# Performance work log

Hardware: AMD Instinct MI355X
Metric: run time of the kernel (lower is better)

Reference implementation:

```python
import jax, jax.numpy as jnp
import numpy as np

B, N, C, D = 2, 6, 64, 40
FH, FW = 12, 33
IMG_H, IMG_W = 384, 1056
NX, NY, NZ = 100, 100, 4
LOWER = np.array([-50.0, -50.0, -10.0], np.float32)   # xbound[0], ybound[0], zbound[0]
DXV = np.array([1.0, 1.0, 5.0], np.float32)           # voxel sizes


def _conv(x, w, pad):
    return jax.lax.conv_general_dilated(x, w, (1, 1), [(pad, pad), (pad, pad)],
                                        dimension_numbers=('NCHW', 'OIHW', 'NCHW'))


def _bn(x, s, b):
    return x * s[None, :, None, None] + b[None, :, None, None]


def _se(x, w1, b1, w2, b2):
    m = x.mean((2, 3))                                   # global avg pool -> (B, C)
    g = jax.nn.sigmoid(jax.nn.silu(m @ w1.T + b1) @ w2.T + b2)
    return x * g[:, :, None, None]


def _frustum():
    ds = jnp.arange(4.0, 44.0, 1.0)                      # (D,) depth bins
    xs = jnp.linspace(0.0, IMG_W - 1.0, FW)
    ys = jnp.linspace(0.0, IMG_H - 1.0, FH)
    f = jnp.stack(jnp.broadcast_arrays(xs[None, None, :], ys[None, :, None], ds[:, None, None]), -1)
    return f.reshape(-1, 3)                              # (D*FH*FW, 3) in (x_px, y_px, depth)


def reference(feats, rots, trans, intrinsics, nw1, bn1s, bn1b, se1w1, se1b1, se1w2, se1b2,
              nw2, bn2s, bn2b, dhw, dhb, chw, chb, bcw1, bcs1, bcb1, bcsw1, bcsb1, bcsw2,
              bcsb2, bcw2, bcs2, bcb2, dw1, ds1, db1, dw2, db2):
    BN = B * N
    # ---- CamEncoderV2 neck + heads (backbone 1280ch@1/32 features given directly) ----
    x = jax.nn.silu(_bn(_conv(feats, nw1, 0), bn1s, bn1b))
    x = _se(x, se1w1, se1b1, se1w2, se1b2)
    x = jax.nn.silu(_bn(_conv(x, nw2, 1), bn2s, bn2b))
    depth = jax.nn.softmax(_conv(x, dhw, 0) + dhb[None, :, None, None], axis=1)  # (BN, D, FH, FW)
    ctx = _conv(x, chw, 0) + chb[None, :, None, None]                            # (BN, C, FH, FW)
    # ---- geometry: pixel frustum -> ego-frame points ----
    rots_f = rots.reshape(BN, 3, 3)
    trans_f = trans.reshape(BN, 3)
    K = intrinsics.reshape(BN, 3, 3)
    pts = _frustum()                                     # (P0, 3), P0 = D*FH*FW
    d = pts[:, 2]
    fx, fy = K[:, 0, 0][:, None], K[:, 1, 1][:, None]
    cx, cy = K[:, 0, 2][:, None], K[:, 1, 2][:, None]
    cam = jnp.stack([(pts[None, :, 0] - cx) * d[None, :] / fx,
                     (pts[None, :, 1] - cy) * d[None, :] / fy,
                     jnp.broadcast_to(d[None, :], (BN, d.shape[0]))], -1)        # (BN, P0, 3)
    geom = jnp.einsum('bij,bpj->bpi', rots_f, cam) + trans_f[:, None, :]
    geom = geom.reshape(B, -1, 3)                        # (B, N*P0, 3)
    # ---- lift: outer product context x depth ----
    ff = (ctx[:, None, :, :, :] * depth[:, :, None, :, :])                       # (BN, D, C, FH, FW)
    ff = ff.transpose(0, 1, 3, 4, 2).reshape(B, -1, C)                           # (B, N*P0, C)
    # ---- splat: voxel pooling (scatter-add into BEV grid) ----
    idx = jnp.floor((geom - jnp.asarray(LOWER)) / jnp.asarray(DXV)).astype(jnp.int32)
    valid = jnp.all((idx >= 0) & (idx < jnp.array([NX, NY, NZ])), axis=-1)
    sid = idx[..., 2] * (NX * NY) + idx[..., 0] * NY + idx[..., 1]
    sid = jnp.where(valid, sid, 0)
    ffm = ff * valid[..., None]
    pooled = jax.vmap(lambda f, i: jax.ops.segment_sum(f, i, num_segments=NZ * NX * NY))(ffm, sid)
    bev = pooled.reshape(B, NZ, NX, NY, C).transpose(0, 1, 4, 2, 3).reshape(B, NZ * C, NX, NY)
    # ---- BEVCompressorV2 (residual conv-SE-conv) ----
    h = jax.nn.relu(_bn(_conv(bev, bcw1, 1), bcs1, bcb1))
    h = _se(h, bcsw1, bcsb1, bcsw2, bcsb2)
    h = jax.nn.relu(_bn(_conv(h, bcw2, 1), bcs2, bcb2))
    bev = bev + h
    # ---- decoder ----
    h = jax.nn.relu(_bn(_conv(bev, dw1, 1), ds1, db1))
    out = _conv(h, dw2, 0) + db2[None, :, None, None]    # (B, nz*num_classes, NX, NY)
    return out.reshape(B, 4, NZ, NX, NY)


def setup_inputs():
    f32 = jnp.float32
    ks = jax.random.split(jax.random.key(0), 16)
    feats = jax.random.normal(ks[0], (B * N, 1280, FH, FW), f32) * 0.5
    # cam->ego: z_cam -> x_ego, -x_cam -> y_ego, -y_cam -> z_ego, plus per-camera yaw
    Rbase = np.array([[0., 0., 1.], [-1., 0., 0.], [0., -1., 0.]], np.float32)
    yaw = np.deg2rad(np.arange(N) * 60.0).astype(np.float32)
    c, s = np.cos(yaw), np.sin(yaw)
    Rz = np.zeros((N, 3, 3), np.float32)
    Rz[:, 0, 0] = c; Rz[:, 0, 1] = -s; Rz[:, 1, 0] = s; Rz[:, 1, 1] = c; Rz[:, 2, 2] = 1.0
    rots = jnp.asarray(np.broadcast_to(np.einsum('nij,jk->nik', Rz, Rbase), (B, N, 3, 3)).copy())
    trans = jax.random.normal(ks[1], (B, N, 3), f32) * 1.0
    K = np.array([[800., 0., 528.], [0., 800., 192.], [0., 0., 1.]], np.float32)
    intrinsics = jnp.asarray(np.broadcast_to(K, (B, N, 3, 3)).copy())

    def w(k, shape, fan_in):
        return jax.random.normal(k, shape, f32) * np.float32(np.sqrt(2.0 / fan_in))

    kk = jax.random.split(ks[2], 16)
    return dict(
        feats=feats, rots=rots, trans=trans, intrinsics=intrinsics,
        nw1=w(kk[0], (256, 1280, 1, 1), 1280), bn1s=jnp.ones(256, f32), bn1b=jnp.zeros(256, f32),
        se1w1=w(kk[1], (32, 256), 256), se1b1=jnp.zeros(32, f32),
        se1w2=w(kk[2], (256, 32), 32), se1b2=jnp.zeros(256, f32),
        nw2=w(kk[3], (256, 256, 3, 3), 2304), bn2s=jnp.ones(256, f32), bn2b=jnp.zeros(256, f32),
        dhw=w(kk[4], (40, 256, 1, 1), 256), dhb=jnp.zeros(40, f32),
        chw=w(kk[5], (64, 256, 1, 1), 256), chb=jnp.zeros(64, f32),
        bcw1=w(kk[6], (256, 256, 3, 3), 2304), bcs1=jnp.ones(256, f32), bcb1=jnp.zeros(256, f32),
        bcsw1=w(kk[7], (16, 256), 256), bcsb1=jnp.zeros(16, f32),
        bcsw2=w(kk[8], (256, 16), 16), bcsb2=jnp.zeros(256, f32),
        bcw2=w(kk[9], (256, 256, 3, 3), 2304), bcs2=jnp.ones(256, f32), bcb2=jnp.zeros(256, f32),
        dw1=w(kk[10], (128, 256, 3, 3), 2304), ds1=jnp.ones(128, f32), db1=jnp.zeros(128, f32),
        dw2=w(kk[11], (16, 128, 1, 1), 128), db2=jnp.zeros(16, f32),
    )
```

## Files before the change

### kernel.cpp

```cpp
#include <hip/hip_runtime.h>
#include <hip/hip_bf16.h>
#include <cmath>


typedef __attribute__((ext_vector_type(8))) short short8;
typedef __attribute__((ext_vector_type(4))) float floatx4;
typedef __hip_bfloat16 hb;

__device__ __forceinline__ float sigf(float x){ return 1.0f/(1.0f+expf(-x)); }
__device__ __forceinline__ float siluf(float x){ return x*sigf(x); }
__device__ __forceinline__ void split2(float v, hb* h, hb* l){
  hb hv = __float2bfloat16(v);
  *h = hv; *l = __float2bfloat16(v - __bfloat162float(hv));
}

__global__ __launch_bounds__(256) void k_trans_featsP(
    const float* __restrict__ feats, hb* __restrict__ Fph, hb* __restrict__ Fpl)
{
  __shared__ float tile[64][65];
  int n = blockIdx.z;
  int p0 = blockIdx.x*64;
  int c0 = blockIdx.y*64;
  int tid = threadIdx.x;
  int tr = tid >> 6;
  int tc = tid & 63;
  #pragma unroll
  for (int it=0; it<16; ++it){
    int ci = c0 + it*4 + tr;
    int p = p0 + tc;
    float v = 0.f;
    if (p < 396) v = feats[((size_t)n*1280 + ci)*396 + p];
    tile[it*4+tr][tc] = v;
  }
  __syncthreads();
  #pragma unroll
  for (int iter=0; iter<2; ++iter){
    int idx = iter*256 + tid;
    int oc = idx >> 6;
    int pl = idx & 63;
    int p = p0 + pl;
    if (p < 396){
      int P = n*396 + p;
      int T = P >> 4, mm = P & 15;
      int kb = (c0 >> 5) + (oc >> 2);
      int q = oc & 3;
      int lane = q*16 + mm;
      size_t o = (((size_t)T*40 + kb)*64 + lane)*8;
      #pragma unroll
      for (int j=0; j<8; ++j){
        hb hv, lv; split2(tile[oc*8+j][pl], &hv, &lv);
        Fph[o+j] = hv; Fpl[o+j] = lv;
      }
    }
  }
}

__global__ __launch_bounds__(256) void k_wpackE(
    const float* __restrict__ nw1, const float* __restrict__ nw2,
    hb* __restrict__ Wc1h, hb* __restrict__ Wc1l,
    hb* __restrict__ Wc2h, hb* __restrict__ Wc2l)
{
  int i = blockIdx.x*256 + threadIdx.x;
  if (i < 327680){
    int j = i & 7;
    int lane = (i>>3) & 63;
    int t2 = i >> 9;
    int nb = t2 & 15;
    int kb = t2 >> 4;
    int ci = kb*32 + (lane>>4)*8 + j;
    int co = nb*16 + (lane&15);
    hb hv, lv; split2(nw1[(size_t)co*1280 + ci], &hv, &lv);
    Wc1h[i] = hv; Wc1l[i] = lv;
  } else {
    int i2 = i - 327680;
    if (i2 >= 589824) return;
    int j = i2 & 7;
    int t1 = i2 >> 3;
    int lane = t1 & 63;
    int t2 = t1 >> 6;
    int nb = t2 % 16;
    int t3 = t2 / 16;
    int tap = t3 % 9;
    int kb = t3 / 9;
    int ci = kb*32 + (lane>>4)*8 + j;
    int co = nb*16 + (lane&15);
    hb hv, lv; split2(nw2[(size_t)co*2304 + ci*9 + tap], &hv, &lv);
    Wc2h[i2] = hv; Wc2l[i2] = lv;
  }
}

__global__ __launch_bounds__(256) void k_wpackT3(
    const float* __restrict__ bcw1, const float* __restrict__ bcw2,
    const float* __restrict__ dw1,
    hb* __restrict__ W1h, hb* __restrict__ W1l,
    hb* __restrict__ W2h, hb* __restrict__ W2l,
    hb* __restrict__ W3h, hb* __restrict__ W3l)
{
  int gi = blockIdx.x*256 + threadIdx.x;
  const float* W; hb* Wh; hb* Wl; int NB; int i;
  if (gi < 589824){ W = bcw1; Wh = W1h; Wl = W1l; NB = 16; i = gi; }
  else if (gi < 1179648){ W = bcw2; Wh = W2h; Wl = W2l; NB = 16; i = gi - 589824; }
  else if (gi < 1474560){ W = dw1; Wh = W3h; Wl = W3l; NB = 8; i = gi - 1179648; }
  else return;
  int j = i & 7;
  int t1 = i >> 3;
  int lane = t1 & 63;
  int t2 = t1 >> 6;
  int nb = t2 % NB;
  int t3 = t2 / NB;
  int tap = t3 % 9;
  int kb = t3 / 9;
  int ci = kb*32 + (lane>>4)*8 + j;
  int co = nb*16 + (lane&15);
  hb hv, lv; split2(W[(size_t)co*2304 + ci*9 + tap], &hv, &lv);
  Wh[i] = hv; Wl[i] = lv;
}

__global__ __launch_bounds__(256) void k_wpackH(
    const float* __restrict__ dhw, const float* __restrict__ chw,
    hb* __restrict__ Wph, hb* __restrict__ Wpl)
{
  int i = blockIdx.x*256 + threadIdx.x;
  if (i >= 8*7*512) return;
  int j = i & 7;
  int t1 = i >> 3;
  int lane = t1 & 63;
  int t2 = t1 >> 6;
  int nb = t2 % 7;
  int kb = t2 / 7;
  int ci = kb*32 + (lane>>4)*8 + j;
  int co = nb*16 + (lane&15);
  float w = 0.f;
  if (co < 40) w = dhw[(size_t)co*256 + ci];
  else if (co < 104) w = chw[(size_t)(co-40)*256 + ci];
  hb hv, lv; split2(w, &hv, &lv);
  Wph[i] = hv; Wpl[i] = lv;
}

__global__ __launch_bounds__(256) void k_mfma_gemm1(
    const hb* __restrict__ Fph, const hb* __restrict__ Fpl,
    const hb* __restrict__ Wph, const hb* __restrict__ Wpl,
    const float* __restrict__ bns, const float* __restrict__ bnb,
    float* __restrict__ out)
{
  __shared__ short8 lbh[256], lbl[256];
  int tid = threadIdx.x;
  int wv = tid >> 6, lane = tid & 63;
  int cog = blockIdx.y;
  int Pbase = blockIdx.x*128 + wv*32;
  int q = lane >> 4;
  int T0 = blockIdx.x*8 + wv*2; if (T0 > 296) T0 = 296;
  int T1 = T0 + 1;              if (T1 > 296) T1 = 296;
  size_t a0 = (size_t)T0*2560 + lane;
  size_t a1 = (size_t)T1*2560 + lane;
  const short8* gAh = (const short8*)(const void*)Fph;
  const short8* gAl = (const short8*)(const void*)Fpl;
  const short8* gWh = (const short8*)(const void*)Wph;
  const short8* gWl = (const short8*)(const void*)Wpl;
  size_t sb = (size_t)(cog*4 + wv)*64 + lane;
  floatx4 acc[2][4];
  #pragma unroll
  for (int i=0;i<2;++i)
    #pragma unroll
    for (int j=0;j<4;++j) acc[i][j] = (floatx4)(0.f);
  short8 ph = gWh[sb], pw = gWl[sb];
  short8 cah0 = gAh[a0], cal0 = gAl[a0], cah1 = gAh[a1], cal1 = gAl[a1];
  for (int kb=0; kb<40; ++kb){
    __syncthreads();
    lbh[tid] = ph; lbl[tid] = pw;
    int nx = (kb+1 < 40) ? kb+1 : 39;
    ph = gWh[(size_t)nx*1024 + sb]; pw = gWl[(size_t)nx*1024 + sb];
    __syncthreads();
    short8 nah0 = gAh[a0 + (size_t)nx*64];
    short8 nal0 = gAl[a0 + (size_t)nx*64];
    short8 nah1 = gAh[a1 + (size_t)nx*64];
    short8 nal1 = gAl[a1 + (size_t)nx*64];
    #pragma unroll
    for (int nb=0; nb<4; ++nb){
      short8 bh = lbh[nb*64 + lane];
      short8 bl = lbl[nb*64 + lane];
      acc[0][nb] = __builtin_amdgcn_mfma_f32_16x16x32_bf16(cah0, bh, acc[0][nb], 0,0,0);
      acc[0][nb] = __builtin_amdgcn_mfma_f32_16x16x32_bf16(cah0, bl, acc[0][nb], 0,0,0);
      acc[0][nb] = __builtin_amdgcn_mfma_f32_16x16x32_bf16(cal0, bh, acc[0][nb], 0,0,0);
      acc[1][nb] = __builtin_amdgcn_mfma_f32_16x16x32_bf16(cah1, bh, acc[1][nb], 0,0,0);
      acc[1][nb] = __builtin_amdgcn_mfma_f32_16x16x32_bf16(cah1, bl, acc[1][nb], 0,0,0);
      acc[1][nb] = __builtin_amdgcn_mfma_f32_16x16x32_bf16(cal1, bh, acc[1][nb], 0,0,0);
    }
    cah0 = nah0; cal0 = nal0; cah1 = nah1; cal1 = nal1;
  }
  int n16 = lane & 15;
  #pragma unroll
  for (int mg=0; mg<2; ++mg){
    #pragma unroll
    for (int nb=0; nb<4; ++nb){
      int co = cog*64 + nb*16 + n16;
      float s = bns[co], bv = bnb[co];
      #pragma unroll
      for (int r=0; r<4; ++r){
        int P = Pbase + mg*16 + q*4 + r;
        if (P < 4752) out[(size_t)P*256 + co] = siluf(acc[mg][nb][r]*s + bv);
      }
    }
  }
}

__global__ __launch_bounds__(256) void k_meanse(
    const float* __restrict__ x1, const float* __restrict__ w1, const float* __restrict__ b1,
    const float* __restrict__ w2, const float* __restrict__ b2, float* __restrict__ g)
{
  __shared__ float m[256];
  __shared__ float h[32];
  int n = blockIdx.x; int t = threadIdx.x;
  float s = 0.f;
  for (int p=0; p<396; ++p) s += x1[((size_t)n*396+p)*256 + t];
  m[t] = s*(1.f/396.f);
  __syncthreads();
  if (t < 32){
    float s2 = b1[t];
    for (int c=0; c<256; ++c) s2 += m[c]*w1[t*256+c];
    h[t] = siluf(s2);
  }
  __syncthreads();
  float s3 = b2[t];
  for (int j=0; j<32; ++j) s3 += h[j]*w2[t*32+j];
  g[n*256+t] = sigf(s3);
}

__global__ __launch_bounds__(256) void k_se_fc(
    const float* __restrict__ mean, const float* __restrict__ w1, const float* __restrict__ b1,
    const float* __restrict__ w2, const float* __restrict__ b2, float* __restrict__ g, int H)
{
  __shared__ float m[256];
  __shared__ float h[32];
  int n = blockIdx.x; int t = threadIdx.x;
  m[t] = mean[n*256 + t];
  __syncthreads();
  if (t < H){
    float s = b1[t];
    for (int c=0; c<256; ++c) s += m[c]*w1[t*256+c];
    h[t] = siluf(s);
  }
  __syncthreads();
  float s = b2[t];
  for (int j=0; j<H; ++j) s += h[j]*w2[t*H+j];
  g[n*256+t] = sigf(s);
}

__global__ __launch_bounds__(256) void k_topad(
    const float* __restrict__ x1, const float* __restrict__ g,
    hb* __restrict__ Xh, hb* __restrict__ Xl)
{
  int y = blockIdx.x;
  int n = blockIdx.y;
  int c = threadIdx.x;
  float gc = g[n*256+c];
  for (int xx=0; xx<35; ++xx){
    float v = 0.f;
    if (y>=1 && y<=12 && xx>=1 && xx<=33)
      v = x1[((size_t)n*396 + (y-1)*33 + (xx-1))*256 + c]*gc;
    hb hv, lv; split2(v, &hv, &lv);
    size_t o = (((size_t)n*14+y)*35+xx)*256 + c;
    Xh[o] = hv; Xl[o] = lv;
  }
}

__global__ __launch_bounds__(256) void k_conv3_img(
    const hb* __restrict__ Xh, const hb* __restrict__ Xl,
    const hb* __restrict__ Wph, const hb* __restrict__ Wpl,
    const float* __restrict__ bns, const float* __restrict__ bnb,
    hb* __restrict__ outh, hb* __restrict__ outl)
{
  __shared__ __align__(16) short sAh[10*18*44];
  __shared__ __align__(16) short sAl[10*18*44];
  __shared__ short8 lbh[2][256], lbl[2][256];
  int tid = threadIdx.x;
  int wv = tid >> 6, lane = tid & 63;
  int xg = blockIdx.x;
  int n = blockIdx.y >> 1, yg = blockIdx.y & 1;
  int cog = blockIdx.z;
  int x0 = xg*16;
  int y0 = yg*8 + wv;
  int m = lane & 15, q = lane >> 4;
  floatx4 acc[2][4];
  #pragma unroll
  for (int i=0;i<2;++i)
    #pragma unroll
    for (int j=0;j<4;++j) acc[i][j] = (floatx4)(0.f);

  const short8* gAh = (const short8*)(const void*)Xh;
  const short8* gAl = (const short8*)(const void*)Xl;
  const short8* gWh = (const short8*)(const void*)Wph;
  const short8* gWl = (const short8*)(const void*)Wpl;
  const size_t sb = (size_t)(cog*4 + wv)*64 + lane;
  const size_t nbase = (size_t)n*14*35*32;

  short8 ph = gWh[sb], pl = gWl[sb];
  int cur = 0;

  for (int kb=0; kb<8; ++kb){
    #pragma unroll 3
    for (int tap=0; tap<9; ++tap){
      int idx2 = kb*9 + tap;
      if (tap == 0){
        __syncthreads();
        for (int i = tid; i < 720; i += 256){
          int rc = i >> 2, part = i & 3;
          int r = rc / 18, c2 = rc % 18;
          int yr = yg*8 + r; if (yr > 13) yr = 13;
          int xc = x0 + c2;  if (xc > 34) xc = 34;
          size_t so = nbase + (size_t)(yr*35 + xc)*32 + kb*4 + part;
          short8 vh = gAh[so], vl = gAl[so];
          int dst = (r*18 + c2)*44 + part*8;
          *(short8*)(sAh + dst) = vh;
          *(short8*)(sAl + dst) = vl;
        }
      }
      lbh[cur][tid] = ph; lbl[cur][tid] = pl;
      int nx = (idx2+1 < 72) ? idx2+1 : 71;
      ph = gWh[(size_t)nx*1024 + sb];
      pl = gWl[(size_t)nx*1024 + sb];
      __syncthreads();
      int dy = (tap*11) >> 5;
      int dx = tap - dy*3;
      int cc = dx + m;
      int a0 = ((wv + dy)*18 + cc)*44 + q*8;
      int a1 = ((wv + 4 + dy)*18 + cc)*44 + q*8;
      short8 cah0 = *(const short8*)(sAh + a0);
      short8 cal0 = *(const short8*)(sAl + a0);
      short8 cah1 = *(const short8*)(sAh + a1);
      short8 cal1 = *(const short8*)(sAl + a1);
      #pragma unroll
      for (int nb=0; nb<4; ++nb){
        short8 bh = lbh[cur][nb*64 + lane];
        short8 bl = lbl[cur][nb*64 + lane];
        acc[0][nb] = __builtin_amdgcn_mfma_f32_16x16x32_bf16(cah0, bh, acc[0][nb], 0,0,0);
        acc[0][nb] = __builtin_amdgcn_mfma_f32_16x16x32_bf16(cah0, bl, acc[0][nb], 0,0,0);
        acc[0][nb] = __builtin_amdgcn_mfma_f32_16x16x32_bf16(cal0, bh, acc[0][nb], 0,0,0);
        acc[1][nb] = __builtin_amdgcn_mfma_f32_16x16x32_bf16(cah1, bh, acc[1][nb], 0,0,0);
        acc[1][nb] = __builtin_amdgcn_mfma_f32_16x16x32_bf16(cah1, bl, acc[1][nb], 0,0,0);
        acc[1][nb] = __builtin_amdgcn_mfma_f32_16x16x32_bf16(cal1, bh, acc[1][nb], 0,0,0);
      }
      cur ^= 1;
    }
  }

  int n16 = lane & 15;
  #pragma unroll
  for (int mg=0; mg<2; ++mg){
    int oy = y0 + mg*4;
    if (oy < 12){
      #pragma unroll
      for (int r=0; r<4; ++r){
        int ox = x0 + q*4 + r;
        if (ox < 33){
          int P = n*396 + oy*33 + ox;
          #pragma unroll
          for (int nb=0; nb<4; ++nb){
            int co = cog*64 + nb*16 + n16;
            float v = siluf(acc[mg][nb][r]*bns[co] + bnb[co]);
            hb hv, lv; split2(v, &hv, &lv);
            outh[(size_t)P*256 + co] = hv;
            outl[(size_t)P*256 + co] = lv;
          }
        }
      }
    }
  }
}

__global__ __launch_bounds__(256) void k_headsM(
    const hb* __restrict__ x2h, const hb* __restrict__ x2l,
    const hb* __restrict__ Whh, const hb* __restrict__ Whl,
    const float* __restrict__ dhb, const float* __restrict__ chb,
    float* __restrict__ dep, float* __restrict__ ctx2)
{
  __shared__ short8 lbh[256], lbl[256];
  int tid = threadIdx.x;
  int wv = tid >> 6, lane = tid & 63;
  int cog = blockIdx.y;
  int nb0 = cog*4;
  int nbN = cog ? 3 : 4;
  int Pbase = blockIdx.x*128 + wv*32;
  int m = lane & 15, q = lane >> 4;
  int P0 = Pbase + m;      if (P0 > 4751) P0 = 4751;
  int P1 = Pbase + 16 + m; if (P1 > 4751) P1 = 4751;
  size_t rA0 = (size_t)P0*32 + q;
  size_t rA1 = (size_t)P1*32 + q;
  const short8* gAh = (const short8*)(const void*)x2h;
  const short8* gAl = (const short8*)(const void*)x2l;
  const short8* gWh = (const short8*)(const void*)Whh;
  const short8* gWl = (const short8*)(const void*)Whl;
  floatx4 acc[2][4];
  #pragma unroll
  for (int i=0;i<2;++i)
    #pragma unroll
    for (int j=0;j<4;++j) acc[i][j] = (floatx4)(0.f);
  for (int kb=0; kb<8; ++kb){
    __syncthreads();
    for (int i=tid; i<nbN*64; i+=256){
      lbh[i] = gWh[(size_t)(kb*7 + nb0)*64 + i];
      lbl[i] = gWl[(size_t)(kb*7 + nb0)*64 + i];
    }
    __syncthreads();
    short8 ah0 = gAh[rA0 + kb*4], al0 = gAl[rA0 + kb*4];
    short8 ah1 = gAh[rA1 + kb*4], al1 = gAl[rA1 + kb*4];
    for (int nb=0; nb<nbN; ++nb){
      short8 bh = lbh[nb*64 + lane];
      short8 bl = lbl[nb*64 + lane];
      acc[0][nb] = __builtin_amdgcn_mfma_f32_16x16x32_bf16(ah0, bh, acc[0][nb], 0,0,0);
      acc[0][nb] = __builtin_amdgcn_mfma_f32_16x16x32_bf16(ah0, bl, acc[0][nb], 0,0,0);
      acc[0][nb] = __builtin_amdgcn_mfma_f32_16x16x32_bf16(al0, bh, acc[0][nb], 0,0,0);
      acc[1][nb] = __builtin_amdgcn_mfma_f32_16x16x32_bf16(ah1, bh, acc[1][nb], 0,0,0);
      acc[1][nb] = __builtin_amdgcn_mfma_f32_16x16x32_bf16(ah1, bl, acc[1][nb], 0,0,0);
      acc[1][nb] = __builtin_amdgcn_mfma_f32_16x16x32_bf16(al1, bh, acc[1][nb], 0,0,0);
    }
  }
  int n16 = lane & 15;
  #pragma unroll
  for (int mg=0; mg<2; ++mg){
    #pragma unroll
    for (int r=0; r<4; ++r){
      int P = Pbase + mg*16 + q*4 + r;
      if (P < 4752){
        int nn = P/396, pim = P%396;
        for (int nb=0; nb<nbN; ++nb){
          int co = cog*64 + nb*16 + n16;
          float v = acc[mg][nb][r];
          if (co < 40)
            dep[((size_t)nn*40 + co)*396 + pim] = v + dhb[co];
          else if (co < 104)
            ctx2[((size_t)nn*396 + pim)*64 + (co-40)] = v + chb[co-40];
        }
      }
    }
  }
}

__global__ __launch_bounds__(256) void k_softmax40(float* __restrict__ dep)
{
  int i = blockIdx.x*256 + threadIdx.x;
  if (i >= 12*396) return;
  int n = i/396, p = i%396;
  float* base = dep + (size_t)n*40*396 + p;
  float mx = -1e30f;
  for (int d=0; d<40; ++d) mx = fmaxf(mx, base[(size_t)d*396]);
  float s = 0.f;
  for (int d=0; d<40; ++d){ float e = expf(base[(size_t)d*396]-mx); base[(size_t)d*396]=e; s+=e; }
  float inv = 1.f/s;
  for (int d=0; d<40; ++d) base[(size_t)d*396] *= inv;
}

__global__ __launch_bounds__(256) void k_geom(
    const float* __restrict__ rots, const float* __restrict__ trans,
    const float* __restrict__ intr, int* __restrict__ vox, int* __restrict__ cnt)
{
  int pt = blockIdx.x*256 + threadIdx.x;
  if (pt >= 190080) return;
  int b = pt/95040; int r = pt%95040;
  int n = r/15840;  int r2 = r%15840;
  int d = r2/396;   int pim = r2%396;
  int y = pim/33, x = pim%33;
  int bn = b*6+n;
  const float* R = rots + (size_t)bn*9;
  const float* T = trans + (size_t)bn*3;
  const float* K = intr + (size_t)bn*9;
  float fx=K[0], cx=K[2], fy=K[4], cy=K[5];
  float xs = (float)x * 32.96875f;
  float ys = (float)((double)y * (383.0/11.0));
  float dv = 4.0f + (float)d;
  float camx = (xs-cx)*dv/fx;
  float camy = (ys-cy)*dv/fy;
  float gx = R[0]*camx + R[1]*camy + R[2]*dv + T[0];
  float gy = R[3]*camx + R[4]*camy + R[5]*dv + T[1];
  float gz = R[6]*camx + R[7]*camy + R[8]*dv + T[2];
  int ix = (int)floorf(gx + 50.f);
  int iy = (int)floorf(gy + 50.f);
  int iz = (int)floorf((gz + 10.f)/5.f);
  bool valid = (ix>=0 && ix<100 && iy>=0 && iy<100 && iz>=0 && iz<4);
  int sid = iz*10000 + ix*100 + iy;
  vox[pt] = valid ? sid : -1;
  if (valid) atomicAdd(&cnt[b*40000 + sid], 1);
}

__global__ __launch_bounds__(256) void k_scan1(
    const int* __restrict__ cnt, int* __restrict__ off, int* __restrict__ bsum)
{
  __shared__ int s[256];
  int t = threadIdx.x;
  int i = blockIdx.x*256 + t;
  int v = (i < 80000) ? cnt[i] : 0;
  s[t] = v; __syncthreads();
  for (int o=1;o<256;o<<=1){
    int x = (t>=o) ? s[t-o] : 0;
    __syncthreads();
    s[t] += x;
    __syncthreads();
  }
  if (i < 80000) off[i] = s[t] - v;
  if (t == 255) bsum[blockIdx.x] = s[255];
}

__global__ void k_scan2(int* __restrict__ bsum, int nblk)
{
  if (threadIdx.x==0 && blockIdx.x==0){
    int run = 0;
    for (int j=0;j<nblk;++j){ int t = bsum[j]; bsum[j] = run; run += t; }
  }
}

__global__ __launch_bounds__(256) void k_scan3(
    int* __restrict__ off, const int* __restrict__ bsum, int* __restrict__ cur)
{
  int i = blockIdx.x*256 + threadIdx.x;
  if (i >= 80000) return;
  int o = off[i] + bsum[i>>8];
  off[i] = o;
  cur[i] = o;
}

__global__ __launch_bounds__(256) void k_fill(
    const int* __restrict__ vox, int* __restrict__ cur, int* __restrict__ list)
{
  int pt = blockIdx.x*256 + threadIdx.x;
  if (pt >= 190080) return;
  int s = vox[pt];
  if (s < 0) return;
  int b = pt/95040;
  int slot = atomicAdd(&cur[b*40000 + s], 1);
  list[slot] = pt;
}

__global__ __launch_bounds__(256) void k_zero_ring(hb* __restrict__ Ah, hb* __restrict__ Al)
{
  int i = blockIdx.x*256 + threadIdx.x;
  if (i >= 2*404*256) return;
  int c = i & 255;
  int t = i >> 8;
  int b = t / 404;
  int ridx = t % 404;
  int py, px;
  if (ridx < 102){ py = 0; px = ridx; }
  else if (ridx < 204){ py = 101; px = ridx-102; }
  else if (ridx < 304){ py = ridx-204+1; px = 0; }
  else { py = ridx-304+1; px = 101; }
  size_t o = (((size_t)b*102 + py)*102 + px)*256 + c;
  hb z = __float2bfloat16(0.f);
  Ah[o] = z; Al[o] = z;
}

__global__ __launch_bounds__(256) void k_gather(
    const int* __restrict__ off, const int* __restrict__ cnt, const int* __restrict__ list,
    const float* __restrict__ ctx2, const float* __restrict__ dep, float* __restrict__ bev,
    hb* __restrict__ Ah, hb* __restrict__ Al)
{
  int tid = threadIdx.x;
  int bv = blockIdx.x*4 + (tid>>6);
  int c = tid & 63;
  int b = bv/40000, sid = bv%40000;
  int st = off[bv], nn = cnt[bv];
  float s = 0.f;
  for (int k=0;k<nn;++k){
    int pt = list[st+k];
    int r = pt%95040;
    int bn = b*6 + r/15840;
    int r2 = r%15840;
    int dd = r2/396, pim = r2%396;
    s += ctx2[((size_t)bn*396+pim)*64 + c] * dep[((size_t)bn*40+dd)*396 + pim];
  }
  int iz = sid/10000, rem = sid%10000;
  bev[(size_t)b*2560000 + (size_t)iz*640000 + (size_t)c*10000 + rem] = s;
  int ix = rem/100, iy = rem%100;
  size_t oh = (((size_t)b*102 + (ix+1))*102 + (iy+1))*256 + iz*64 + c;
  hb hv, lv; split2(s, &hv, &lv);
  Ah[oh] = hv; Al[oh] = lv;
}

__global__ __launch_bounds__(256) void k_tohwc2(
    const float* __restrict__ in, hb* __restrict__ Ah, hb* __restrict__ Al,
    const float* __restrict__ g)
{
  __shared__ float tile[32*105];
  int py = blockIdx.x;
  int b  = blockIdx.y;
  int cg = blockIdx.z;
  int tid = threadIdx.x;
  bool inner = (py >= 1 && py <= 100);
  if (inner){
    if (tid < 64){ int cil = tid & 31; int col = (tid>>5) ? 101 : 0; tile[cil*105 + col] = 0.f; }
    for (int i = tid; i < 3200; i += 256){
      int cil = i / 100, x = i % 100;
      int ci = cg*32 + cil;
      tile[cil*105 + (x+1)] = in[(((size_t)b*256 + ci)*100 + (py-1))*100 + x];
    }
  }
  __syncthreads();
  for (int i = tid; i < 32*102; i += 256){
    int px = i >> 5, cil = i & 31;
    int ci = cg*32 + cil;
    float v = 0.f;
    if (inner){
      v = tile[cil*105 + px];
      if (g) v *= g[b*256 + ci];
    }
    hb hv, lv; split2(v, &hv, &lv);
    size_t o = (((size_t)b*102 + py)*102 + px)*256 + ci;
    Ah[o] = hv; Al[o] = lv;
  }
}

__global__ __launch_bounds__(256) void k_rowmean(
    const float* __restrict__ in, float* __restrict__ out, int rowlen, float inv)
{
  __shared__ float ws[4];
  int row = blockIdx.x; int t = threadIdx.x;
  const float* p = in + (size_t)row*rowlen;
  float s = 0.f;
  for (int i=t; i<rowlen; i+=256) s += p[i];
  #pragma unroll
  for (int off=32; off; off>>=1) s += __shfl_down(s, off);
  if ((t&63)==0) ws[t>>6] = s;
  __syncthreads();
  if (t==0) out[row] = (ws[0]+ws[1]+ws[2]+ws[3]) * inv;
}

__global__ __launch_bounds__(256) void k_conv3_bevm(
    const hb* __restrict__ Ah, const hb* __restrict__ Al,
    const hb* __restrict__ Wph, const hb* __restrict__ Wpl,
    const float* __restrict__ bns, const float* __restrict__ bnb,
    const float* __restrict__ res, float* __restrict__ out, int Cout, int NBG)
{
  __shared__ __align__(16) short sAh[10*18*44];
  __shared__ __align__(16) short sAl[10*18*44];
  __shared__ short8 lbh[2][256], lbl[2][256];
  const int NB = Cout >> 4;
  int tid = threadIdx.x;
  int wv = tid >> 6, lane = tid & 63;
  int L = blockIdx.x;
  int spatial = L / (NBG*2);
  int rem = L % (NBG*2);
  int cog = rem % NBG;
  int bb  = rem / NBG;
  int xg = spatial % 7, yg = spatial / 7;
  int x0 = xg*16;
  int y0 = yg*8 + wv;
  int m = lane & 15, q = lane >> 4;
  int nb0 = cog*4;
  floatx4 acc[2][4];
  #pragma unroll
  for (int i=0;i<2;++i)
    #pragma unroll
    for (int j=0;j<4;++j) acc[i][j] = (floatx4)(0.f);

  const short8* gAh = (const short8*)(const void*)Ah;
  const short8* gAl = (const short8*)(const void*)Al;
  const short8* gWh = (const short8*)(const void*)Wph;
  const short8* gWl = (const short8*)(const void*)Wpl;
  const size_t nbstride = (size_t)NB*64;
  const size_t sb = (size_t)(nb0 + wv)*64 + lane;

  short8 ph = gWh[sb], pl = gWl[sb];
  int cur = 0;

  for (int kb=0; kb<8; ++kb){
    #pragma unroll 3
    for (int tap=0; tap<9; ++tap){
      int idx2 = kb*9 + tap;
      if (tap == 0){
        __syncthreads();
        for (int i = tid; i < 720; i += 256){
          int rc = i >> 2, part = i & 3;
          int r = rc / 18, c = rc % 18;
          int yr = yg*8 + r; if (yr > 101) yr = 101;
          int xc = x0 + c;   if (xc > 101) xc = 101;
          size_t so = ((size_t)((bb*102 + yr)*102 + xc))*32 + kb*4 + part;
          short8 vh = gAh[so], vl = gAl[so];
          int dst = (r*18 + c)*44 + part*8;
          *(short8*)(sAh + dst) = vh;
          *(short8*)(sAl + dst) = vl;
        }
      }
      lbh[cur][tid] = ph; lbl[cur][tid] = pl;
      int nx = (idx2+1 < 72) ? idx2+1 : 71;
      ph = gWh[(size_t)nx*nbstride + sb];
      pl = gWl[(size_t)nx*nbstride + sb];
      __syncthreads();
      int dy = (tap*11) >> 5;
      int dx = tap - dy*3;
      int cc = dx + m;
      int a0 = ((wv + dy)*18 + cc)*44 + q*8;
      int a1 = ((wv + 4 + dy)*18 + cc)*44 + q*8;
      short8 cah0 = *(const short8*)(sAh + a0);
      short8 cal0 = *(const short8*)(sAl + a0);
      short8 cah1 = *(const short8*)(sAh + a1);
      short8 cal1 = *(const short8*)(sAl + a1);
      #pragma unroll
      for (int nb=0; nb<4; ++nb){
        short8 bh = lbh[cur][nb*64 + lane];
        short8 bl = lbl[cur][nb*64 + lane];
        acc[0][nb] = __builtin_amdgcn_mfma_f32_16x16x32_bf16(cah0, bh, acc[0][nb], 0,0,0);
        acc[0][nb] = __builtin_amdgcn_mfma_f32_16x16x32_bf16(cah0, bl, acc[0][nb], 0,0,0);
        acc[0][nb] = __builtin_amdgcn_mfma_f32_16x16x32_bf16(cal0, bh, acc[0][nb], 0,0,0);
        acc[1][nb] = __builtin_amdgcn_mfma_f32_16x16x32_bf16(cah1, bh, acc[1][nb], 0,0,0);
        acc[1][nb] = __builtin_amdgcn_mfma_f32_16x16x32_bf16(cah1, bl, acc[1][nb], 0,0,0);
        acc[1][nb] = __builtin_amdgcn_mfma_f32_16x16x32_bf16(cal1, bh, acc[1][nb], 0,0,0);
      }
      cur ^= 1;
    }
  }

  int n = lane & 15;
  int xq = x0 + q*4;
  #pragma unroll
  for (int mg=0; mg<2; ++mg){
    int yo = y0 + mg*4;
    if (yo < 100 && xq < 100){
      #pragma unroll
      for (int nb=0; nb<4; ++nb){
        int co = cog*64 + nb*16 + n;
        float s = bns[co], bv = bnb[co];
        floatx4 a = acc[mg][nb];
        float4 v;
        v.x = fmaxf(a[0]*s+bv, 0.f);
        v.y = fmaxf(a[1]*s+bv, 0.f);
        v.z = fmaxf(a[2]*s+bv, 0.f);
        v.w = fmaxf(a[3]*s+bv, 0.f);
        size_t o = ((size_t)(bb*Cout+co)*100 + yo)*100 + xq;
        if (res){
          float4 rv = *(const float4*)(res + o);
          v.x += rv.x; v.y += rv.y; v.z += rv.z; v.w += rv.w;
        }
        *(float4*)(out + o) = v;
      }
    }
  }
}

__global__ __launch_bounds__(256) void k_final2(
    const float* __restrict__ h, const float* __restrict__ W, const float* __restrict__ bias,
    float* __restrict__ out)
{
  __shared__ float wsl[2048];
  __shared__ float bs[16];
  int tid = threadIdx.x;
  int b = blockIdx.y;
  for (int i=tid; i<2048; i+=256) wsl[i] = W[i];
  if (tid < 16) bs[tid] = bias[tid];
  __syncthreads();
  int pix = blockIdx.x*256 + tid;
  if (pix >= 10000) return;
  float acc[16];
  #pragma unroll
  for (int oc=0; oc<16; ++oc) acc[oc] = bs[oc];
  const float* hb_ = h + (size_t)b*128*10000 + pix;
  for (int ci=0; ci<128; ++ci){
    float hv = hb_[(size_t)ci*10000];
    #pragma unroll
    for (int oc=0; oc<16; ++oc) acc[oc] += hv * wsl[oc*128 + ci];
  }
  #pragma unroll
  for (int oc=0; oc<16; ++oc)
    out[((size_t)(b*16+oc))*10000 + pix] = acc[oc];
}

extern "C" void kernel_launch(void* const* d_in, const int* in_sizes, int n_in,
                              void* d_out, int out_size, void* d_ws, size_t ws_size,
                              hipStream_t stream)
{
  (void)in_sizes; (void)n_in; (void)out_size; (void)ws_size;
  const float* feats = (const float*)d_in[0];
  const float* rots  = (const float*)d_in[1];
  const float* trans = (const float*)d_in[2];
  const float* intr  = (const float*)d_in[3];
  const float* nw1   = (const float*)d_in[4];
  const float* bn1s  = (const float*)d_in[5];
  const float* bn1b  = (const float*)d_in[6];
  const float* se1w1 = (const float*)d_in[7];
  const float* se1b1 = (const float*)d_in[8];
  const float* se1w2 = (const float*)d_in[9];
  const float* se1b2 = (const float*)d_in[10];
  const float* nw2   = (const float*)d_in[11];
  const float* bn2s  = (const float*)d_in[12];
  const float* bn2b  = (const float*)d_in[13];
  const float* dhw   = (const float*)d_in[14];
  const float* dhb   = (const float*)d_in[15];
  const float* chw   = (const float*)d_in[16];
  const float* chb   = (const float*)d_in[17];
  const float* bcw1  = (const float*)d_in[18];
  const float* bcs1  = (const float*)d_in[19];
  const float* bcb1  = (const float*)d_in[20];
  const float* bcsw1 = (const float*)d_in[21];
  const float* bcsb1 = (const float*)d_in[22];
  const float* bcsw2 = (const float*)d_in[23];
  const float* bcsb2 = (const float*)d_in[24];
  const float* bcw2  = (const float*)d_in[25];
  const float* bcs2  = (const float*)d_in[26];
  const float* bcb2  = (const float*)d_in[27];
  const float* dw1   = (const float*)d_in[28];
  const float* ds1   = (const float*)d_in[29];
  const float* db1   = (const float*)d_in[30];
  const float* dw2   = (const float*)d_in[31];
  const float* db2   = (const float*)d_in[32];
  float* out = (float*)d_out;

  float* ws = (float*)d_ws;
  float* bev   = ws;
  float* h1    = ws + 5120000;
  hb*    Ah    = (hb*)(ws + 10240000);
  hb*    Al    = (hb*)(ws + 12903424);
  float* x2    = ws + 15566848;
  float* S5    = ws + 16783360;
  float* dep   = ws + 17373184;
  float* ctx2  = ws + 17563264;
  float* mean1 = ws + 17867392;
  float* g1    = mean1 + 3072;
  float* mean2 = g1 + 3072;
  float* g2    = mean2 + 512;
  int*   vox   = (int*)(ws + 17875584);
  hb* Fph  = (hb*)bev;
  hb* Wc1h = (hb*)(bev + 3041280);
  hb* Wc1l = (hb*)(bev + 3205120);
  float* x1 = h1;
  hb* Fpl  = (hb*)(h1 + 1216512);
  hb* Xh   = (hb*)Ah;
  hb* Xl   = (hb*)Al;
  hb* Wc2h = (hb*)S5;
  hb* Wc2l = (hb*)(S5 + 294912);
  hb* x2h  = (hb*)x2;
  hb* x2l  = (hb*)(x2 + 608256);
  hb* Whh  = (hb*)S5;
  hb* Whl  = (hb*)(S5 + 14336);
  int* cnt  = (int*)h1;
  int* off  = cnt + 80000;
  int* cur  = off + 80000;
  int* bsum = cur + 80000;
  int* list = bsum + 1024;
  float* h3 = h1;
  hb* Wp1h = (hb*)x2;
  hb* Wp1l = (hb*)(x2 + 294912);
  hb* Wp3h = (hb*)(x2 + 589824);
  hb* Wp3l = (hb*)(x2 + 589824 + 147456);
  hb* Wp2h = (hb*)S5;
  hb* Wp2l = (hb*)(S5 + 294912);

  k_trans_featsP<<<dim3(7,20,12),256,0,stream>>>(feats,Fph,Fpl);
  k_wpackE<<<3584,256,0,stream>>>(nw1,nw2,Wc1h,Wc1l,Wc2h,Wc2l);
  k_mfma_gemm1<<<dim3(38,4),256,0,stream>>>(Fph,Fpl,Wc1h,Wc1l,bn1s,bn1b,x1);
  k_meanse<<<12,256,0,stream>>>(x1,se1w1,se1b1,se1w2,se1b2,g1);
  k_topad<<<dim3(14,12),256,0,stream>>>(x1,g1,Xh,Xl);
  k_conv3_img<<<dim3(3,24,4),256,0,stream>>>(Xh,Xl,Wc2h,Wc2l,bn2s,bn2b,x2h,x2l);
  k_wpackH<<<112,256,0,stream>>>(dhw,chw,Whh,Whl);
  k_headsM<<<dim3(38,2),256,0,stream>>>(x2h,x2l,Whh,Whl,dhb,chb,dep,ctx2);
  k_softmax40<<<19,256,0,stream>>>(dep);

  k_wpackT3<<<5760,256,0,stream>>>(bcw1,bcw2,dw1,Wp1h,Wp1l,Wp2h,Wp2l,Wp3h,Wp3l);

  hipMemsetAsync(cnt, 0, 80000*sizeof(int), stream);
  k_geom<<<(190080+255)/256,256,0,stream>>>(rots,trans,intr,vox,cnt);
  k_scan1<<<313,256,0,stream>>>(cnt,off,bsum);
  k_scan2<<<1,64,0,stream>>>(bsum,313);
  k_scan3<<<(80000+255)/256,256,0,stream>>>(off,bsum,cur);
  k_fill<<<(190080+255)/256,256,0,stream>>>(vox,cur,list);
  k_zero_ring<<<808,256,0,stream>>>(Ah,Al);
  k_gather<<<20000,256,0,stream>>>(off,cnt,list,ctx2,dep,bev,Ah,Al);

  k_conv3_bevm<<<728,256,0,stream>>>(Ah,Al,Wp1h,Wp1l,bcs1,bcb1,nullptr,h1,256,4);
  k_rowmean<<<512,256,0,stream>>>(h1,mean2,10000,1e-4f);
  k_se_fc<<<2,256,0,stream>>>(mean2,bcsw1,bcsb1,bcsw2,bcsb2,g2,16);
  k_tohwc2<<<dim3(102,2,8),256,0,stream>>>(h1,Ah,Al,g2);
  k_conv3_bevm<<<728,256,0,stream>>>(Ah,Al,Wp2h,Wp2l,bcs2,bcb2,bev,bev,256,4);
  k_tohwc2<<<dim3(102,2,8),256,0,stream>>>(bev,Ah,Al,nullptr);
  k_conv3_bevm<<<364,256,0,stream>>>(Ah,Al,Wp3h,Wp3l,ds1,db1,nullptr,h3,128,2);
  k_final2<<<dim3(40,2),256,0,stream>>>(h3,dw2,db2,out);
}
```

Measured before the change: 671.5 us.

## Split conv3 BEV waves by channel pairs, drop LDS weight staging; warp-parallel block scan

The 3x3 BEV conv kernel now gives each wave 4 output rows by 2 channel blocks, so each wave loads its own weight fragments straight from global into registers. This removes the LDS weight double-buffer and the per-tap __syncthreads. The trade-off is more redundant global weight loads and more activation LDS reads per wave. The single-thread serial scan over block sums is also replaced by a 64-lane shuffle scan.

```diff
diff --git a/kernel.cpp b/kernel.cpp
--- a/kernel.cpp
+++ b/kernel.cpp
@@ -502,9 +502,20 @@
 
 __global__ void k_scan2(int* __restrict__ bsum, int nblk)
 {
-  if (threadIdx.x==0 && blockIdx.x==0){
-    int run = 0;
-    for (int j=0;j<nblk;++j){ int t = bsum[j]; bsum[j] = run; run += t; }
+  int lane = threadIdx.x & 63;
+  int run = 0;
+  for (int base=0; base<nblk; base+=64){
+    int i = base + lane;
+    int v = (i < nblk) ? bsum[i] : 0;
+    int s = v;
+    #pragma unroll
+    for (int o=1;o<64;o<<=1){
+      int t = __shfl_up(s, o);
+      if (lane >= o) s += t;
+    }
+    int total = __shfl(s, 63);
+    if (i < nblk) bsum[i] = run + s - v;
+    run += total;
   }
 }
 
@@ -631,10 +642,11 @@
 {
   __shared__ __align__(16) short sAh[10*18*44];
   __shared__ __align__(16) short sAl[10*18*44];
-  __shared__ short8 lbh[2][256], lbl[2][256];
   const int NB = Cout >> 4;
   int tid = threadIdx.x;
   int wv = tid >> 6, lane = tid & 63;
+  int wc = wv & 1;
+  int wy = wv >> 1;
   int L = blockIdx.x;
   int spatial = L / (NBG*2);
   int rem = L % (NBG*2);
@@ -642,83 +654,81 @@
   int bb  = rem / NBG;
   int xg = spatial % 7, yg = spatial / 7;
   int x0 = xg*16;
-  int y0 = yg*8 + wv;
   int m = lane & 15, q = lane >> 4;
-  int nb0 = cog*4;
-  floatx4 acc[2][4];
-  #pragma unroll
-  for (int i=0;i<2;++i)
+  int nb0 = cog*4 + wc*2;
+  floatx4 acc[4][2];
+  #pragma unroll
+  for (int r=0;r<4;++r)
     #pragma unroll
-    for (int j=0;j<4;++j) acc[i][j] = (floatx4)(0.f);
+    for (int u=0;u<2;++u) acc[r][u] = (floatx4)(0.f);
 
   const short8* gAh = (const short8*)(const void*)Ah;
   const short8* gAl = (const short8*)(const void*)Al;
   const short8* gWh = (const short8*)(const void*)Wph;
   const short8* gWl = (const short8*)(const void*)Wpl;
   const size_t nbstride = (size_t)NB*64;
-  const size_t sb = (size_t)(nb0 + wv)*64 + lane;
-
-  short8 ph = gWh[sb], pl = gWl[sb];
-  int cur = 0;
+
+  short8 pbh[2], pbl[2];
+  #pragma unroll
+  for (int u=0;u<2;++u){
+    pbh[u] = gWh[(size_t)(nb0+u)*64 + lane];
+    pbl[u] = gWl[(size_t)(nb0+u)*64 + lane];
+  }
 
   for (int kb=0; kb<8; ++kb){
+    __syncthreads();
+    for (int i = tid; i < 720; i += 256){
+      int rc = i >> 2, part = i & 3;
+      int r = rc / 18, c = rc % 18;
+      int yr = yg*8 + r; if (yr > 101) yr = 101;
+      int xc = x0 + c;   if (xc > 101) xc = 101;
+      size_t so = ((size_t)((bb*102 + yr)*102 + xc))*32 + kb*4 + part;
+      short8 vh = gAh[so], vl = gAl[so];
+      int dst = (r*18 + c)*44 + part*8;
+      *(short8*)(sAh + dst) = vh;
+      *(short8*)(sAl + dst) = vl;
+    }
+    __syncthreads();
     #pragma unroll 3
     for (int tap=0; tap<9; ++tap){
       int idx2 = kb*9 + tap;
-      if (tap == 0){
-        __syncthreads();
-        for (int i = tid; i < 720; i += 256){
-          int rc = i >> 2, part = i & 3;
-          int r = rc / 18, c = rc % 18;
-          int yr = yg*8 + r; if (yr > 101) yr = 101;
-          int xc = x0 + c;   if (xc > 101) xc = 101;
-          size_t so = ((size_t)((bb*102 + yr)*102 + xc))*32 + kb*4 + part;
-          short8 vh = gAh[so], vl = gAl[so];
-          int dst = (r*18 + c)*44 + part*8;
-          *(short8*)(sAh + dst) = vh;
-          *(short8*)(sAl + dst) = vl;
-        }
+      short8 cbh0 = pbh[0], cbh1 = pbh[1];
+      short8 cbl0 = pbl[0], cbl1 = pbl[1];
+      int nx = (idx2+1 < 72) ? idx2+1 : 71;
+      #pragma unroll
+      for (int u=0;u<2;++u){
+        pbh[u] = gWh[(size_t)nx*nbstride + (size_t)(nb0+u)*64 + lane];
+        pbl[u] = gWl[(size_t)nx*nbstride + (size_t)(nb0+u)*64 + lane];
       }
-      lbh[cur][tid] = ph; lbl[cur][tid] = pl;
-      int nx = (idx2+1 < 72) ? idx2+1 : 71;
-      ph = gWh[(size_t)nx*nbstride + sb];
-      pl = gWl[(size_t)nx*nbstride + sb];
-      __syncthreads();
       int dy = (tap*11) >> 5;
       int dx = tap - dy*3;
       int cc = dx + m;
-      int a0 = ((wv + dy)*18 + cc)*44 + q*8;
-      int a1 = ((wv + 4 + dy)*18 + cc)*44 + q*8;
-      short8 cah0 = *(const short8*)(sAh + a0);
-      short8 cal0 = *(const short8*)(sAl + a0);
-      short8 cah1 = *(const short8*)(sAh + a1);
-      short8 cal1 = *(const short8*)(sAl + a1);
       #pragma unroll
-      for (int nb=0; nb<4; ++nb){
-        short8 bh = lbh[cur][nb*64 + lane];
-        short8 bl = lbl[cur][nb*64 + lane];
-        acc[0][nb] = __builtin_amdgcn_mfma_f32_16x16x32_bf16(cah0, bh, acc[0][nb], 0,0,0);
-        acc[0][nb] = __builtin_amdgcn_mfma_f32_16x16x32_bf16(cah0, bl, acc[0][nb], 0,0,0);
-        acc[0][nb] = __builtin_amdgcn_mfma_f32_16x16x32_bf16(cal0, bh, acc[0][nb], 0,0,0);
-        acc[1][nb] = __builtin_amdgcn_mfma_f32_16x16x32_bf16(cah1, bh, acc[1][nb], 0,0,0);
-        acc[1][nb] = __builtin_amdgcn_mfma_f32_16x16x32_bf16(cah1, bl, acc[1][nb], 0,0,0);
-        acc[1][nb] = __builtin_amdgcn_mfma_f32_16x16x32_bf16(cal1, bh, acc[1][nb], 0,0,0);
+      for (int r=0; r<4; ++r){
+        int a0 = ((wy*4 + r + dy)*18 + cc)*44 + q*8;
+        short8 cah = *(const short8*)(sAh + a0);
+        short8 cal = *(const short8*)(sAl + a0);
+        acc[r][0] = __builtin_amdgcn_mfma_f32_16x16x32_bf16(cah, cbh0, acc[r][0], 0,0,0);
+        acc[r][0] = __builtin_amdgcn_mfma_f32_16x16x32_bf16(cah, cbl0, acc[r][0], 0,0,0);
+        acc[r][0] = __builtin_amdgcn_mfma_f32_16x16x32_bf16(cal, cbh0, acc[r][0], 0,0,0);
+        acc[r][1] = __builtin_amdgcn_mfma_f32_16x16x32_bf16(cah, cbh1, acc[r][1], 0,0,0);
+        acc[r][1] = __builtin_amdgcn_mfma_f32_16x16x32_bf16(cah, cbl1, acc[r][1], 0,0,0);
+        acc[r][1] = __builtin_amdgcn_mfma_f32_16x16x32_bf16(cal, cbh1, acc[r][1], 0,0,0);
       }
-      cur ^= 1;
     }
   }
 
   int n = lane & 15;
   int xq = x0 + q*4;
   #pragma unroll
-  for (int mg=0; mg<2; ++mg){
-    int yo = y0 + mg*4;
+  for (int r=0; r<4; ++r){
+    int yo = yg*8 + wy*4 + r;
     if (yo < 100 && xq < 100){
       #pragma unroll
-      for (int nb=0; nb<4; ++nb){
-        int co = cog*64 + nb*16 + n;
+      for (int u=0; u<2; ++u){
+        int co = (nb0+u)*16 + n;
         float s = bns[co], bv = bnb[co];
-        floatx4 a = acc[mg][nb];
+        floatx4 a = acc[r][u];
         float4 v;
         v.x = fmaxf(a[0]*s+bv, 0.f);
         v.y = fmaxf(a[1]*s+bv, 0.f);
```

After: 631.4 us. 1.06x faster.
